# Kernel tuning notes

Measured on AMD Instinct MI355X. Metric: run time of the kernel, lower is better.

## Reference

```python
import jax, jax.numpy as jnp
import numpy as np

N_HEAD = 16
THETA = 10000.0


def _freqs_cos_sin(head_dim, seq_len):
    # matches precompute_freqs_cis: freqs = 1/theta^(arange(0,dim,2)/dim), outer with t
    inv = 1.0 / (THETA ** (jnp.arange(0, head_dim, 2, dtype=jnp.float32) / head_dim))
    t = jnp.arange(seq_len, dtype=jnp.float32)
    ang = jnp.outer(t, inv)  # [L, head_dim//2]
    return jnp.cos(ang), jnp.sin(ang)


def _rope(x, cos, sin):
    # x: [B, H, L, D]; pairs are interleaved (view_as_complex on (..., D//2, 2))
    x1 = x[..., 0::2]
    x2 = x[..., 1::2]
    out_re = x1 * cos - x2 * sin
    out_im = x1 * sin + x2 * cos
    return jnp.stack([out_re, out_im], axis=-1).reshape(x.shape)


def setup_inputs() -> dict:
    key = jax.random.key(0)
    ks = jax.random.split(key, 11)
    B, L, D = 2, 2048, 1024
    s = 0.02
    return {
        "q": jax.random.normal(ks[0], (B, L, D), jnp.float32),
        "k": jax.random.normal(ks[1], (B, L, D), jnp.float32),
        "v": jax.random.normal(ks[2], (B, L, D), jnp.float32),
        "wq": jax.random.normal(ks[3], (D, D), jnp.float32) * s,
        "bq": jax.random.normal(ks[4], (D,), jnp.float32) * s,
        "wk": jax.random.normal(ks[5], (D, D), jnp.float32) * s,
        "bk": jax.random.normal(ks[6], (D,), jnp.float32) * s,
        "wv": jax.random.normal(ks[7], (D, D), jnp.float32) * s,
        "bv": jax.random.normal(ks[8], (D,), jnp.float32) * s,
        "wo": jax.random.normal(ks[9], (D, D), jnp.float32) * s,
        "bo": jax.random.normal(ks[10], (D,), jnp.float32) * s,
    }


def reference(q, k, v, wq, bq, wk, bk, wv, bv, wo, bo):
    B, L, D = q.shape
    Hd = D // N_HEAD
    # projections (nn.Linear: x @ W^T + b)
    qp = q @ wq.T + bq
    kp = k @ wk.T + bk
    vp = v @ wv.T + bv
    # split: [B, L, D] -> [B, H, L, Hd]
    def split(t):
        return t.reshape(B, L, N_HEAD, Hd).transpose(0, 2, 1, 3)
    qh, kh, vh = split(qp), split(kp), split(vp)
    cos, sin = _freqs_cos_sin(Hd, L)  # [L, Hd//2], broadcasts over B, H
    qh = _rope(qh, cos, sin)
    kh = _rope(kh, cos, sin)
    # scaled dot-product attention (no mask)
    scores = jnp.einsum("bhqd,bhkd->bhqk", qh, kh) / jnp.sqrt(jnp.float32(Hd))
    attn = jax.nn.softmax(scores, axis=-1)
    out = jnp.einsum("bhqk,bhkd->bhqd", attn, vh)
    # concat heads and output projection
    out = out.transpose(0, 2, 1, 3).reshape(B, L, D)
    return out @ wo.T + bo
```

## Files before the change

### kernel.cpp

```cpp
#include <hip/hip_runtime.h>
#include <hip/hip_bf16.h>
#include <math.h>

#define BB 2
#define LL 2048
#define DD 1024
#define NH 16
#define HD 64

typedef short v8s __attribute__((ext_vector_type(8)));
typedef float v4f __attribute__((ext_vector_type(4)));
typedef float v16f __attribute__((ext_vector_type(16)));

__device__ __forceinline__ float b2f(unsigned short b) {
  union { unsigned int u; float f; } c; c.u = ((unsigned int)b) << 16; return c.f;
}
__device__ __forceinline__ unsigned short f2b(float x) {
  union { float f; unsigned int u; } c; c.f = x;
  unsigned int u = c.u;
  u += 0x7fffu + ((u >> 16) & 1u);
  return (unsigned short)(u >> 16);
}
__device__ __forceinline__ unsigned int asu(float x) {
  union { float f; unsigned int u; } c; c.f = x; return c.u;
}
__device__ __forceinline__ unsigned int pk2(float lo, float hi) {
  return __builtin_amdgcn_perm(asu(hi), asu(lo), 0x07060302u);
}

#if defined(__has_builtin)
#if __has_builtin(__builtin_amdgcn_exp2f)
#define EXP2(x) __builtin_amdgcn_exp2f(x)
#else
#define EXP2(x) __expf((x) * 0.69314718056f)
#endif
#else
#define EXP2(x) __expf((x) * 0.69314718056f)
#endif

__device__ __forceinline__ void gload16(const void* g, void* l) {
  __builtin_amdgcn_global_load_lds(
      (const __attribute__((address_space(1))) void*)g,
      (__attribute__((address_space(3))) void*)l, 16, 0, 0);
}

#define VM_WAIT4 do { asm volatile("s_waitcnt vmcnt(4)" ::: "memory"); \
                      __builtin_amdgcn_sched_barrier(0); } while (0)
#define VM_WAIT0 do { asm volatile("s_waitcnt vmcnt(0)" ::: "memory"); \
                      __builtin_amdgcn_sched_barrier(0); } while (0)
#define SBAR     do { __builtin_amdgcn_s_barrier(); \
                      __builtin_amdgcn_sched_barrier(0); } while (0)

struct CastArgs { const float* s[7]; unsigned short* d[7]; float* ct; float* st; };
__global__ void cast_all(CastArgs a) {
  int z = blockIdx.z;
  if (z == 16) {
    if (blockIdx.x >= 256) return;
    int id = blockIdx.x * blockDim.x + threadIdx.x;
    int t = id >> 5, i = id & 31;
    float inv = powf(10000.0f, -(float)(2 * i) / 64.0f);
    float ang = (float)t * inv;
    a.ct[id] = cosf(ang);
    a.st[id] = sinf(ang);
    return;
  }
  int t = (z < 12) ? (z >> 2) : (z - 9);
  int off = (z < 12) ? ((z & 3) << 18) : 0;
  int i = off + blockIdx.x * blockDim.x + threadIdx.x;
  float4 v = ((const float4*)a.s[t])[i];
  ushort4 o;
  o.x = f2b(v.x); o.y = f2b(v.y); o.z = f2b(v.z); o.w = f2b(v.w);
  ((ushort4*)a.d[t])[i] = o;
}

__device__ __forceinline__ size_t ring_src_off(int id, int row0, int Kd) {
  int sr = id >> 3, slot = id & 7;
  int g = slot ^ (sr & 7);
  int r = (sr << 1) | (g >> 2), c = g & 3;
  return (size_t)(row0 + r) * Kd + c * 8;
}
__device__ __forceinline__ int ring_frag_off(int row, int quad) {
  int sr = row >> 1;
  int slot = (((row & 1) << 2) | quad) ^ (sr & 7);
  return sr * 64 + slot * 8;
}

__device__ __forceinline__ void ring_gemm_core(
    const unsigned short* __restrict__ X, const unsigned short* __restrict__ W,
    unsigned short* LDS_, int bm0, int bn0, v4f acc[4][4]) {
  const int K = DD;
  const int tid = threadIdx.x;
  const int lane = tid & 63, wave = tid >> 6;
  const int quad = lane >> 4, l16 = lane & 15;
  const int wm = (wave >> 1) * 64, wn = (wave & 1) * 64;

  const unsigned short* aS0 = X + ring_src_off(tid, bm0, K);
  const unsigned short* aS1 = X + ring_src_off(256 + tid, bm0, K);
  const unsigned short* bS0 = W + ring_src_off(tid, bn0, K);
  const unsigned short* bS1 = W + ring_src_off(256 + tid, bn0, K);

  int aoff[4], boff[4];
#pragma unroll
  for (int i = 0; i < 4; ++i) {
    aoff[i] = ring_frag_off(wm + i * 16 + l16, quad);
    boff[i] = ring_frag_off(wn + i * 16 + l16, quad);
  }

  auto stage = [&](int q, int kofs) {
    unsigned short* Ab = &LDS_[q * 4096];
    unsigned short* Bb = &LDS_[12288 + q * 4096];
    gload16(aS0 + kofs, &Ab[tid * 8]);
    gload16(aS1 + kofs, &Ab[(256 + tid) * 8]);
    gload16(bS0 + kofs, &Bb[tid * 8]);
    gload16(bS1 + kofs, &Bb[(256 + tid) * 8]);
  };
  auto compute = [&](int q) {
    const unsigned short* Ab = &LDS_[q * 4096];
    const unsigned short* Bb = &LDS_[12288 + q * 4096];
    v8s a[4], b[4];
#pragma unroll
    for (int i = 0; i < 4; ++i) {
      a[i] = *(const v8s*)&Ab[aoff[i]];
      b[i] = *(const v8s*)&Bb[boff[i]];
    }
#pragma unroll
    for (int mi = 0; mi < 4; ++mi)
#pragma unroll
      for (int ni = 0; ni < 4; ++ni)
        acc[mi][ni] = __builtin_amdgcn_mfma_f32_16x16x32_bf16(a[mi], b[ni], acc[mi][ni], 0, 0, 0);
  };

  const int nt = K / 32;
  stage(0, 0);
  stage(1, 32);
  VM_WAIT4;
  SBAR;
  int cur = 0, s2 = 2, kofs = 64;
#pragma unroll 1
  for (int t = 0; t < nt - 2; ++t) {
    stage(s2, kofs);
    compute(cur);
    VM_WAIT4;
    SBAR;
    cur = (cur == 2) ? 0 : cur + 1;
    s2 = (s2 == 2) ? 0 : s2 + 1;
    kofs += 32;
  }
  compute(cur);
  VM_WAIT0;
  SBAR;
  cur = (cur == 2) ? 0 : cur + 1;
  compute(cur);
}

__global__ __launch_bounds__(256, 3) void gemm_qkv(
    const unsigned short* __restrict__ qb, const unsigned short* __restrict__ kb,
    const unsigned short* __restrict__ vb,
    const unsigned short* __restrict__ wqb, const unsigned short* __restrict__ wkb,
    const unsigned short* __restrict__ wvb,
    const float* __restrict__ bq, const float* __restrict__ bk,
    const float* __restrict__ bv_,
    unsigned short* __restrict__ qp, unsigned short* __restrict__ khh,
    unsigned short* __restrict__ vt,
    const float* __restrict__ ctab, const float* __restrict__ stab) {
  __shared__ __align__(16) unsigned short LDS_[24576];
  const int z = blockIdx.z;
  const unsigned short* X = (z == 0) ? qb : (z == 1) ? kb : vb;
  const unsigned short* W = (z == 0) ? wqb : (z == 1) ? wkb : wvb;
  const float* bias = (z == 0) ? bq : (z == 1) ? bk : bv_;
  const int N = DD;
  const int tid = threadIdx.x;
  const int lane = tid & 63, wave = tid >> 6;
  const int quad = lane >> 4, l16 = lane & 15;
  const int bm0 = blockIdx.x * 128;
  const int bn0 = blockIdx.y * 128;
  const int wm = (wave >> 1) * 64, wn = (wave & 1) * 64;

  const v4f vzero = {0.f, 0.f, 0.f, 0.f};
  v4f acc[4][4];
#pragma unroll
  for (int i = 0; i < 4; ++i)
#pragma unroll
    for (int j = 0; j < 4; ++j) acc[i][j] = vzero;

  ring_gemm_core(X, W, LDS_, bm0, bn0, acc);

  float bv[4];
#pragma unroll
  for (int ni = 0; ni < 4; ++ni) bv[ni] = bias[bn0 + wn + ni * 16 + l16];

  if (z < 2) {
    const float scl = (z == 0) ? 0.18033688f : 1.0f;
    const int h = (bn0 + wn) >> 6;
    const float sgn = (l16 & 1) ? 1.0f : -1.0f;
#pragma unroll
    for (int mi = 0; mi < 4; ++mi) {
#pragma unroll
      for (int r = 0; r < 4; ++r) {
        int row = bm0 + wm + mi * 16 + quad * 4 + r;
        int l = row & (LL - 1);
        int bidx = row >> 11;
        size_t baseq = (size_t)row * N + bn0 + wn + l16;
        size_t basek = ((size_t)(bidx * NH + h) * LL + l) * HD + l16;
#pragma unroll
        for (int ni = 0; ni < 4; ++ni) {
          int ii = (ni * 16 + l16) >> 1;
          float c = ctab[l * 32 + ii], s = stab[l * 32 + ii];
          float v = acc[mi][ni][r] + bv[ni];
          float vp = __shfl_xor(v, 1);
          float o = (v * c + sgn * (vp * s)) * scl;
          if (z == 0) qp[baseq + ni * 16] = f2b(o);
          else        khh[basek + ni * 16] = f2b(o);
        }
      }
    }
  } else {
    __syncthreads();
    unsigned short* T = LDS_;
#pragma unroll
    for (int mi = 0; mi < 4; ++mi)
#pragma unroll
      for (int r = 0; r < 4; ++r) {
        int tl = wm + mi * 16 + quad * 4 + r;
        int tlp = (tl & ~12) | ((tl & 4) << 1) | ((tl & 8) >> 1);
        int chunk = tlp >> 3, offw = tlp & 7;
#pragma unroll
        for (int ni = 0; ni < 4; ++ni) {
          int fl = wn + ni * 16 + l16;
          T[fl * 128 + ((chunk ^ (fl & 15)) * 8) + offw] =
              f2b(acc[mi][ni][r] + bv[ni]);
        }
      }
    __syncthreads();
    int fl = tid >> 1, half = tid & 1;
    int fg = bn0 + fl;
    int h2 = fg >> 6, d = fg & 63;
    int bidx = bm0 >> 11, l0 = bm0 & (LL - 1);
    unsigned short* dst =
        vt + (((size_t)(bidx * NH + h2) * HD + d) * LL) + l0 + half * 64;
#pragma unroll
    for (int i = 0; i < 8; ++i) {
      int chunk = half * 8 + i;
      int slot = chunk ^ (fl & 15);
      *(v8s*)(dst + i * 8) = *(const v8s*)&T[fl * 128 + slot * 8];
    }
  }
}

__global__ __launch_bounds__(256, 3) void gemm_out(
    const unsigned short* __restrict__ x, const unsigned short* __restrict__ w,
    const float* __restrict__ b, float* __restrict__ y) {
  __shared__ __align__(16) unsigned short LDS_[24576];
  const int N = DD;
  const int tid = threadIdx.x;
  const int lane = tid & 63, wave = tid >> 6;
  const int quad = lane >> 4, l16 = lane & 15;
  const int bm0 = blockIdx.x * 128;
  const int bn0 = blockIdx.y * 128;
  const int wm = (wave >> 1) * 64, wn = (wave & 1) * 64;

  const v4f vzero = {0.f, 0.f, 0.f, 0.f};
  v4f acc[4][4];
#pragma unroll
  for (int i = 0; i < 4; ++i)
#pragma unroll
    for (int j = 0; j < 4; ++j) acc[i][j] = vzero;

  ring_gemm_core(x, w, LDS_, bm0, bn0, acc);

  float bv[4];
#pragma unroll
  for (int ni = 0; ni < 4; ++ni) bv[ni] = b[bn0 + wn + ni * 16 + l16];
#pragma unroll
  for (int mi = 0; mi < 4; ++mi) {
#pragma unroll
    for (int r = 0; r < 4; ++r) {
      int row = bm0 + wm + mi * 16 + quad * 4 + r;
      size_t base = (size_t)row * N + bn0 + wn + l16;
#pragma unroll
      for (int ni = 0; ni < 4; ++ni)
        y[base + ni * 16] = acc[mi][ni][r] + bv[ni];
    }
  }
}

__global__ __launch_bounds__(256, 2) void flash_kernel(
    const unsigned short* __restrict__ qp,
    const unsigned short* __restrict__ kh,
    const unsigned short* __restrict__ vt,
    unsigned short* __restrict__ attn) {
  __shared__ __align__(16) unsigned short S_[2][16384];
  const int tid = threadIdx.x, wave = tid >> 6, lane = tid & 63;
  const int l32 = lane & 31, hf = lane >> 5;
  const int bh = blockIdx.x, b = bh >> 4, hd = bh & 15;
  const int q0 = blockIdx.y * 128;
  const unsigned short* kbase = kh + (size_t)bh * LL * HD;
  const unsigned short* vbase = vt + (size_t)bh * HD * LL;

  const int qrow = q0 + wave * 32 + l32;
  v8s qf[4];
  {
    const unsigned short* qsrc = qp + ((size_t)(b * LL + qrow) * DD + hd * HD);
#pragma unroll
    for (int ks2 = 0; ks2 < 4; ++ks2)
      qf[ks2] = *(const v8s*)(qsrc + ks2 * 16 + hf * 8);
  }

  v16f o0, o1;
#pragma unroll
  for (int i = 0; i < 16; ++i) { o0[i] = 0.0f; o1[i] = 0.0f; }
  float ls = 0.0f;

  {
    unsigned short* Kb = S_[0];
    unsigned short* Vb = S_[0] + 8192;
#pragma unroll
    for (int i = 0; i < 4; ++i) {
      int id = i * 256 + tid;
      int r = id >> 3, c = (id & 7) ^ (r & 7);
      gload16(kbase + (size_t)r * HD + c * 8, &Kb[id * 8]);
    }
#pragma unroll
    for (int i = 0; i < 4; ++i) {
      int id = i * 256 + tid;
      int r = id >> 4, c = (id & 15) ^ (r & 15);
      gload16(vbase + (size_t)r * LL + c * 8, &Vb[id * 8]);
    }
  }

  for (int t = 0; t < 16; ++t) {
    __syncthreads();
    if (t < 15) {
      int kt = (t + 1) * 128;
      unsigned short* Kb = S_[(t + 1) & 1];
      unsigned short* Vb = Kb + 8192;
#pragma unroll
      for (int i = 0; i < 4; ++i) {
        int id = i * 256 + tid;
        int r = id >> 3, c = (id & 7) ^ (r & 7);
        gload16(kbase + (size_t)(kt + r) * HD + c * 8, &Kb[id * 8]);
      }
#pragma unroll
      for (int i = 0; i < 4; ++i) {
        int id = i * 256 + tid;
        int r = id >> 4, c = (id & 15) ^ (r & 15);
        gload16(vbase + (size_t)r * LL + kt + c * 8, &Vb[id * 8]);
      }
    }
    const unsigned short* Ks = S_[t & 1];
    const unsigned short* Vs = Ks + 8192;

#pragma unroll
    for (int g = 0; g < 4; ++g) {
      v16f sc;
#pragma unroll
      for (int i = 0; i < 16; ++i) sc[i] = 0.0f;
#pragma unroll
      for (int ks2 = 0; ks2 < 4; ++ks2) {
        int row = g * 32 + l32;
        int slot = (ks2 * 2 + hf) ^ (lane & 7);
        v8s kf = *(const v8s*)&Ks[row * 64 + slot * 8];
        sc = __builtin_amdgcn_mfma_f32_32x32x16_bf16(kf, qf[ks2], sc, 0, 0, 0);
      }
      v16f e;
#pragma unroll
      for (int i = 0; i < 16; ++i) e[i] = EXP2(sc[i]);
      float t0 = (e[0] + e[1]) + (e[2] + e[3]);
      float t1 = (e[4] + e[5]) + (e[6] + e[7]);
      float t2 = (e[8] + e[9]) + (e[10] + e[11]);
      float t3 = (e[12] + e[13]) + (e[14] + e[15]);
      ls += (t0 + t1) + (t2 + t3);
#pragma unroll
      for (int k2 = 0; k2 < 2; ++k2) {
        union { v8s v; unsigned int u[4]; } pb;
#pragma unroll
        for (int a = 0; a < 4; ++a)
          pb.u[a] = pk2(e[8 * k2 + 2 * a], e[8 * k2 + 2 * a + 1]);
        int k16 = g * 2 + k2;
        int slotv = (k16 * 2 + hf) ^ (lane & 15);
        v8s vf0 = *(const v8s*)&Vs[l32 * 128 + slotv * 8];
        v8s vf1 = *(const v8s*)&Vs[(32 + l32) * 128 + slotv * 8];
        o0 = __builtin_amdgcn_mfma_f32_32x32x16_bf16(vf0, pb.v, o0, 0, 0, 0);
        o1 = __builtin_amdgcn_mfma_f32_32x32x16_bf16(vf1, pb.v, o1, 0, 0, 0);
      }
    }
  }

  ls += __shfl_xor(ls, 32);
  float inv = 1.0f / ls;

  unsigned short* Wt = S_[0] + wave * 2048;
#pragma unroll
  for (int dt = 0; dt < 2; ++dt)
#pragma unroll
    for (int r = 0; r < 16; ++r) {
      int dl = (r & 3) + 8 * (r >> 2) + 4 * hf;
      int d = dt * 32 + dl;
      int chunk = d >> 3, offw = d & 7;
      int slot = chunk ^ (l32 & 7);
      float val = (dt == 0) ? o0[r] : o1[r];
      Wt[l32 * 64 + slot * 8 + offw] = f2b(val * inv);
    }
#pragma unroll
  for (int i = 0; i < 4; ++i) {
    int qr = lane >> 1;
    int chunk = (lane & 1) * 4 + i;
    int slot = chunk ^ (qr & 7);
    v8s dv = *(const v8s*)&Wt[qr * 64 + slot * 8];
    int token = q0 + wave * 32 + qr;
    *(v8s*)(attn + ((size_t)(b * LL + token) * DD) + hd * HD + chunk * 8) = dv;
  }
}

extern "C" void kernel_launch(void* const* d_in, const int* in_sizes, int n_in,
                              void* d_out, int out_size, void* d_ws, size_t ws_size,
                              hipStream_t stream) {
  const float* q  = (const float*)d_in[0];
  const float* k  = (const float*)d_in[1];
  const float* v  = (const float*)d_in[2];
  const float* wq = (const float*)d_in[3];
  const float* bq = (const float*)d_in[4];
  const float* wk = (const float*)d_in[5];
  const float* bk = (const float*)d_in[6];
  const float* wv = (const float*)d_in[7];
  const float* bv = (const float*)d_in[8];
  const float* wo = (const float*)d_in[9];
  const float* bo = (const float*)d_in[10];
  float* out = (float*)d_out;

  size_t off = 0;
  char* wsb = (char*)d_ws;
  auto take = [&](size_t n) { void* p = wsb + off; off += n; return p; };
  const size_t SZT = (size_t)BB * LL * DD * 2;
  const size_t SZW = (size_t)DD * DD * 2;
  unsigned short* qb   = (unsigned short*)take(SZT);
  unsigned short* kb   = (unsigned short*)take(SZT);
  unsigned short* vb   = (unsigned short*)take(SZT);
  unsigned short* wqb  = (unsigned short*)take(SZW);
  unsigned short* wkb  = (unsigned short*)take(SZW);
  unsigned short* wvb  = (unsigned short*)take(SZW);
  unsigned short* wob  = (unsigned short*)take(SZW);
  unsigned short* qp   = (unsigned short*)take(SZT);
  unsigned short* khh  = (unsigned short*)take(SZT);
  unsigned short* vtt  = (unsigned short*)take(SZT);
  unsigned short* attn = (unsigned short*)take(SZT);
  float* ctab = (float*)take((size_t)LL * 32 * 4);
  float* stab = (float*)take((size_t)LL * 32 * 4);

  CastArgs ca;
  ca.s[0] = q;  ca.s[1] = k;  ca.s[2] = v;  ca.s[3] = wq;
  ca.s[4] = wk; ca.s[5] = wv; ca.s[6] = wo;
  ca.d[0] = qb;  ca.d[1] = kb;  ca.d[2] = vb;  ca.d[3] = wqb;
  ca.d[4] = wkb; ca.d[5] = wvb; ca.d[6] = wob;
  ca.ct = ctab; ca.st = stab;
  cast_all<<<dim3(1024, 1, 17), 256, 0, stream>>>(ca);

  gemm_qkv<<<dim3(BB * LL / 128, DD / 128, 3), 256, 0, stream>>>(
      qb, kb, vb, wqb, wkb, wvb, bq, bk, bv, qp, khh, vtt, ctab, stab);

  flash_kernel<<<dim3(BB * NH, LL / 128), 256, 0, stream>>>(
      qp, khh, vtt, attn);

  gemm_out<<<dim3(BB * LL / 128, DD / 128, 1), 256, 0, stream>>>(attn, wob, bo, out);
}
```

Baseline: 211.6 us.

## Triple-buffer 64-key K/V tiles in flash kernel and raise occupancy

Restructures the flash attention main loop to use 64-key tiles in a three-stage LDS ring instead of 128-key double buffering. LDS use drops from 64KB to 48KB and launch bounds rise to 3 blocks per CU. Global addresses are precomputed and waits use explicit vmcnt plus barrier macros, so loads for tile t+2 overlap compute of tile t. The trade-off is more loop iterations, more barriers, and added register pressure from the higher occupancy target.

```diff
diff --git a/kernel.cpp b/kernel.cpp
--- a/kernel.cpp
+++ b/kernel.cpp
@@ -284,12 +284,12 @@
   }
 }
 
-__global__ __launch_bounds__(256, 2) void flash_kernel(
+__global__ __launch_bounds__(256, 3) void flash_kernel(
     const unsigned short* __restrict__ qp,
     const unsigned short* __restrict__ kh,
     const unsigned short* __restrict__ vt,
     unsigned short* __restrict__ attn) {
-  __shared__ __align__(16) unsigned short S_[2][16384];
+  __shared__ __align__(16) unsigned short S_[24576];
   const int tid = threadIdx.x, wave = tid >> 6, lane = tid & 63;
   const int l32 = lane & 31, hf = lane >> 5;
   const int bh = blockIdx.x, b = bh >> 4, hd = bh & 15;
@@ -306,59 +306,39 @@
       qf[ks2] = *(const v8s*)(qsrc + ks2 * 16 + hf * 8);
   }
 
+  const int r0 = tid >> 3, s0 = tid & 7;
+  const int r1 = (256 + tid) >> 3;
+  const unsigned short* kS0 = kbase + (size_t)r0 * HD + (s0 ^ (r0 & 7)) * 8;
+  const unsigned short* kS1 = kbase + (size_t)r1 * HD + (s0 ^ (r1 & 7)) * 8;
+  const unsigned short* vS0 = vbase + (size_t)r0 * LL + (s0 ^ (r0 & 7)) * 8;
+  const unsigned short* vS1 = vbase + (size_t)r1 * LL + (s0 ^ (r1 & 7)) * 8;
+
   v16f o0, o1;
 #pragma unroll
   for (int i = 0; i < 16; ++i) { o0[i] = 0.0f; o1[i] = 0.0f; }
   float ls = 0.0f;
 
-  {
-    unsigned short* Kb = S_[0];
-    unsigned short* Vb = S_[0] + 8192;
-#pragma unroll
-    for (int i = 0; i < 4; ++i) {
-      int id = i * 256 + tid;
-      int r = id >> 3, c = (id & 7) ^ (r & 7);
-      gload16(kbase + (size_t)r * HD + c * 8, &Kb[id * 8]);
-    }
-#pragma unroll
-    for (int i = 0; i < 4; ++i) {
-      int id = i * 256 + tid;
-      int r = id >> 4, c = (id & 15) ^ (r & 15);
-      gload16(vbase + (size_t)r * LL + c * 8, &Vb[id * 8]);
-    }
-  }
-
-  for (int t = 0; t < 16; ++t) {
-    __syncthreads();
-    if (t < 15) {
-      int kt = (t + 1) * 128;
-      unsigned short* Kb = S_[(t + 1) & 1];
-      unsigned short* Vb = Kb + 8192;
-#pragma unroll
-      for (int i = 0; i < 4; ++i) {
-        int id = i * 256 + tid;
-        int r = id >> 3, c = (id & 7) ^ (r & 7);
-        gload16(kbase + (size_t)(kt + r) * HD + c * 8, &Kb[id * 8]);
-      }
-#pragma unroll
-      for (int i = 0; i < 4; ++i) {
-        int id = i * 256 + tid;
-        int r = id >> 4, c = (id & 15) ^ (r & 15);
-        gload16(vbase + (size_t)r * LL + kt + c * 8, &Vb[id * 8]);
-      }
-    }
-    const unsigned short* Ks = S_[t & 1];
-    const unsigned short* Vs = Ks + 8192;
-
-#pragma unroll
-    for (int g = 0; g < 4; ++g) {
+  auto stage = [&](int q, int t) {
+    unsigned short* Kb = &S_[q * 8192];
+    unsigned short* Vb = &S_[q * 8192 + 4096];
+    gload16(kS0 + (size_t)t * 4096, &Kb[tid * 8]);
+    gload16(kS1 + (size_t)t * 4096, &Kb[(256 + tid) * 8]);
+    gload16(vS0 + t * 64, &Vb[tid * 8]);
+    gload16(vS1 + t * 64, &Vb[(256 + tid) * 8]);
+  };
+
+  auto compute = [&](int q) {
+    const unsigned short* Ks = &S_[q * 8192];
+    const unsigned short* Vs = &S_[q * 8192 + 4096];
+#pragma unroll
+    for (int g = 0; g < 2; ++g) {
       v16f sc;
 #pragma unroll
       for (int i = 0; i < 16; ++i) sc[i] = 0.0f;
 #pragma unroll
       for (int ks2 = 0; ks2 < 4; ++ks2) {
         int row = g * 32 + l32;
-        int slot = (ks2 * 2 + hf) ^ (lane & 7);
+        int slot = (ks2 * 2 + hf) ^ (row & 7);
         v8s kf = *(const v8s*)&Ks[row * 64 + slot * 8];
         sc = __builtin_amdgcn_mfma_f32_32x32x16_bf16(kf, qf[ks2], sc, 0, 0, 0);
       }
@@ -377,19 +357,40 @@
         for (int a = 0; a < 4; ++a)
           pb.u[a] = pk2(e[8 * k2 + 2 * a], e[8 * k2 + 2 * a + 1]);
         int k16 = g * 2 + k2;
-        int slotv = (k16 * 2 + hf) ^ (lane & 15);
-        v8s vf0 = *(const v8s*)&Vs[l32 * 128 + slotv * 8];
-        v8s vf1 = *(const v8s*)&Vs[(32 + l32) * 128 + slotv * 8];
+        int slotv = (k16 * 2 + hf) ^ (l32 & 7);
+        v8s vf0 = *(const v8s*)&Vs[l32 * 64 + slotv * 8];
+        v8s vf1 = *(const v8s*)&Vs[(32 + l32) * 64 + slotv * 8];
         o0 = __builtin_amdgcn_mfma_f32_32x32x16_bf16(vf0, pb.v, o0, 0, 0, 0);
         o1 = __builtin_amdgcn_mfma_f32_32x32x16_bf16(vf1, pb.v, o1, 0, 0, 0);
       }
     }
-  }
+  };
+
+  const int nt = LL / 64;
+  stage(0, 0);
+  stage(1, 1);
+  VM_WAIT4;
+  SBAR;
+  int cur = 0, s2 = 2;
+#pragma unroll 1
+  for (int t = 0; t < nt - 2; ++t) {
+    stage(s2, t + 2);
+    compute(cur);
+    VM_WAIT4;
+    SBAR;
+    cur = (cur == 2) ? 0 : cur + 1;
+    s2 = (s2 == 2) ? 0 : s2 + 1;
+  }
+  compute(cur);
+  VM_WAIT0;
+  SBAR;
+  cur = (cur == 2) ? 0 : cur + 1;
+  compute(cur);
 
   ls += __shfl_xor(ls, 32);
   float inv = 1.0f / ls;
 
-  unsigned short* Wt = S_[0] + wave * 2048;
+  unsigned short* Wt = S_ + wave * 2048;
 #pragma unroll
   for (int dt = 0; dt < 2; ++dt)
 #pragma unroll
```

Result: no change. 211.8 us (+0.1%).
